# Performance work log

Measured on AMD Instinct MI355X. Metric: run time of the kernel, lower is better.

Reference implementation:

```python
import jax, jax.numpy as jnp
import numpy as np
from jax import lax

T, N, CIN, CMID, IMG, LABELS = 8, 32, 3, 64, 64, 10
W4 = IMG // 4  # 16 after two 2x2 maxpools
FC1_IN = CMID * W4 * W4                 # 16384
FC1_OUT = (CMID * W4 // 2) * W4 // 2    # 4096 (matches Python int-div precedence)
V_TH = 1.0
ALPHA = 4.0  # spikingjelly surrogate.Sigmoid default alpha

@jax.custom_vjp
def spike(x):
    # Heaviside(v - v_th); surrogate sigmoid gradient in bwd
    return (x >= 0.0).astype(x.dtype)

def _spike_fwd(x):
    return (x >= 0.0).astype(x.dtype), x

def _spike_bwd(x, g):
    s = jax.nn.sigmoid(ALPHA * x)
    return (g * ALPHA * s * (1.0 - s),)

spike.defvjp(_spike_fwd, _spike_bwd)

def if_node(x_seq):
    # IFNode, hard reset to v_reset=0, v starts at 0, multi-step over leading T axis
    def step(v, x):
        v = v + x                 # charge
        s = spike(v - V_TH)       # fire
        return v * (1.0 - s), s   # hard reset (reset path keeps grad: detach_reset=False)
    _, s_seq = lax.scan(step, jnp.zeros_like(x_seq[0]), x_seq)
    return s_seq

def conv2d(x, w):
    # kernel 3x3, stride 1, padding 1, no bias
    return lax.conv_general_dilated(x, w, (1, 1), ((1, 1), (1, 1)),
                                    dimension_numbers=('NCHW', 'OIHW', 'NCHW'))

def maxpool2(x):
    return lax.reduce_window(x, -jnp.inf, lax.max, (1, 1, 2, 2), (1, 1, 2, 2), 'VALID')

def seq_apply(f, x_seq):
    # stateless layer applied over merged [T*N, ...] (spikingjelly step_mode='m')
    t, n = x_seq.shape[:2]
    y = f(x_seq.reshape((t * n,) + x_seq.shape[2:]))
    return y.reshape((t, n) + y.shape[1:])


def setup_inputs() -> dict:
    key = jax.random.key(0)
    k = jax.random.split(key, 5)
    x_seq = jax.random.uniform(k[0], (T, N, CIN, IMG, IMG), dtype=jnp.float32)
    w1 = jax.random.normal(k[1], (CMID, CIN, 3, 3), dtype=jnp.float32) * (1.0 / np.sqrt(CIN * 9))
    w2 = jax.random.normal(k[2], (CMID, CMID, 3, 3), dtype=jnp.float32) * (1.0 / np.sqrt(CMID * 9))
    fc1 = jax.random.normal(k[3], (FC1_OUT, FC1_IN), dtype=jnp.float32) * (1.0 / np.sqrt(FC1_IN))
    fc2 = jax.random.normal(k[4], (LABELS, FC1_OUT), dtype=jnp.float32) * (1.0 / np.sqrt(FC1_OUT))
    return {"x_seq": x_seq, "w1": w1, "w2": w2, "fc1": fc1, "fc2": fc2}


def reference(x_seq, w1, w2, fc1, fc2):
    h = seq_apply(lambda x: conv2d(x, w1), x_seq)   # [T,N,64,64,64]
    h = if_node(h)
    h = seq_apply(maxpool2, h)                      # [T,N,64,32,32]
    h = seq_apply(lambda x: conv2d(x, w2), h)
    h = if_node(h)
    h = seq_apply(maxpool2, h)                      # [T,N,64,16,16]
    h = h.reshape(T, N, -1)                         # [T,N,16384]
    h = if_node(jnp.einsum('tni,oi->tno', h, fc1))  # [T,N,4096]
    h = if_node(jnp.einsum('tni,oi->tno', h, fc2))  # [T,N,10]
    return h.mean(axis=0)                           # firing rate over time: [N,10]
```

## Files before the change

### kernel.cpp

```cpp
#include <hip/hip_runtime.h>
#include <hip/hip_bf16.h>


#define T_STEPS 8
#define NB      32
#define CMID    64

typedef __bf16 bf16x2 __attribute__((ext_vector_type(2)));
typedef __bf16 bf16x4 __attribute__((ext_vector_type(4)));
typedef __bf16 bf16x8 __attribute__((ext_vector_type(8)));
typedef short  s16x8  __attribute__((ext_vector_type(8)));
typedef float  f32x4  __attribute__((ext_vector_type(4)));

struct Split3 { float h, m, l; };
__device__ __forceinline__ Split3 split3(float x) {
    Split3 s;
    __bf16 h = (__bf16)x;
    float r1 = x - (float)h;
    __bf16 m = (__bf16)r1;
    float r2 = r1 - (float)m;
    __bf16 l = (__bf16)r2;
    s.h = (float)h; s.m = (float)m; s.l = (float)l;
    return s;
}

__device__ __forceinline__ void split3v8(float4 a, float4 b,
                                         s16x8& fh, s16x8& fm, s16x8& fl) {
    float x[8] = {a.x, a.y, a.z, a.w, b.x, b.y, b.z, b.w};
    s16x8 h, m, l;
#pragma unroll
    for (int j = 0; j < 8; j++) {
        __bf16 ch = (__bf16)x[j];
        float r1 = x[j] - (float)ch;
        __bf16 cm = (__bf16)r1;
        float r2 = r1 - (float)cm;
        __bf16 cl = (__bf16)r2;
        h[j] = __builtin_bit_cast(short, ch);
        m[j] = __builtin_bit_cast(short, cm);
        l[j] = __builtin_bit_cast(short, cl);
    }
    fh = h; fm = m; fl = l;
}

__device__ __forceinline__ void load_lds16(const void* g, void* l) {
    __builtin_amdgcn_global_load_lds(
        (const __attribute__((address_space(1))) void*)g,
        (__attribute__((address_space(3))) void*)l, 16, 0, 0);
}

__global__ void k_w2s(const float* __restrict__ w2, __bf16* __restrict__ w2s) {
    int idx = blockIdx.x * 256 + threadIdx.x;
    int j    = idx & 7;
    int lane = (idx >> 3) & 63;
    int oh   = (idx >> 9) & 1;
    int kh   = (idx >> 10) & 1;
    int g    = idx >> 11;
    int tap  = g % 9;
    int ch   = g / 9;
    int co = ch * 32 + oh * 16 + (lane & 15);
    int ci = kh * 32 + (lane >> 4) * 8 + j;
    float w = w2[co * 576 + ci * 9 + tap];
    Split3 s = split3(w);
    __bf16* o = w2s + (((size_t)(g * 2 + kh) * 2 + oh) * 3) * 512 + lane * 8 + j;
    o[0]    = (__bf16)s.h;
    o[512]  = (__bf16)s.m;
    o[1024] = (__bf16)s.l;
}

__global__ __launch_bounds__(256) void k_conv1_if_pool(
        const float* __restrict__ x, const float* __restrict__ w1,
        __bf16* __restrict__ spk1p) {
    int b   = blockIdx.x;
    int n   = b >> 5;
    int cog = (b >> 2) & 7;
    int pht = b & 3;
    int tid = threadIdx.x;
    int pw  = tid & 31;
    int ph  = pht * 8 + (tid >> 5);
    int ih0 = 2 * ph - 1, iw0 = 2 * pw - 1;

    float v[8][4];
#pragma unroll
    for (int a = 0; a < 8; a++)
#pragma unroll
        for (int p = 0; p < 4; p++) v[a][p] = 0.f;

    for (int t = 0; t < T_STEPS; t++) {
        const float* xb = x + (size_t)(t * NB + n) * 3 * 4096;
        float patch[3][4][4];
#pragma unroll
        for (int ci = 0; ci < 3; ci++)
#pragma unroll
            for (int dy = 0; dy < 4; dy++) {
                int ih = ih0 + dy;
                bool rok = ((unsigned)ih < 64u);
#pragma unroll
                for (int dx = 0; dx < 4; dx++) {
                    int iw = iw0 + dx;
                    patch[ci][dy][dx] = (rok && ((unsigned)iw < 64u))
                                            ? xb[ci * 4096 + ih * 64 + iw] : 0.f;
                }
            }
        bf16x8 sv;
#pragma unroll
        for (int c8 = 0; c8 < 8; c8++) {
            int co = cog * 8 + c8;
            const float* wc = w1 + co * 27;
            float a0 = 0.f, a1 = 0.f, a2 = 0.f, a3 = 0.f;
#pragma unroll
            for (int ci = 0; ci < 3; ci++)
#pragma unroll
                for (int ky = 0; ky < 3; ky++)
#pragma unroll
                    for (int kx = 0; kx < 3; kx++) {
                        float w = wc[ci * 9 + ky * 3 + kx];
                        a0 += w * patch[ci][ky][kx];
                        a1 += w * patch[ci][ky][kx + 1];
                        a2 += w * patch[ci][ky + 1][kx];
                        a3 += w * patch[ci][ky + 1][kx + 1];
                    }
            float s0, s1, s2, s3;
            v[c8][0] += a0; s0 = (v[c8][0] >= 1.f) ? 1.f : 0.f; if (s0 > 0.f) v[c8][0] = 0.f;
            v[c8][1] += a1; s1 = (v[c8][1] >= 1.f) ? 1.f : 0.f; if (s1 > 0.f) v[c8][1] = 0.f;
            v[c8][2] += a2; s2 = (v[c8][2] >= 1.f) ? 1.f : 0.f; if (s2 > 0.f) v[c8][2] = 0.f;
            v[c8][3] += a3; s3 = (v[c8][3] >= 1.f) ? 1.f : 0.f; if (s3 > 0.f) v[c8][3] = 0.f;
            sv[c8] = (__bf16)fmaxf(fmaxf(s0, s1), fmaxf(s2, s3));
        }
        *(bf16x8*)(spk1p + ((size_t)(t * NB + n) * 1024 + ph * 32 + pw) * 64
                         + cog * 8) = sv;
    }
}

__global__ __launch_bounds__(512, 2) void k_conv2_if_pool(
        const short* __restrict__ spk1p,
        const short* __restrict__ w2s,
        __bf16* __restrict__ spk2) {
    int b     = blockIdx.x;
    int ch    = b & 1;
    int s2    = (b >> 1) & 3;
    int n     = b >> 3;
    int tid   = threadIdx.x;
    int lane  = tid & 63;
    int wv    = tid >> 6;
    int mh    = wv >> 1, oh = wv & 1;
    int lm    = lane & 15, kq = lane >> 4;

    __shared__ short Bs[55296];
    __shared__ short As[10 * 34 * 64];

    {
        const uint4* src = (const uint4*)(w2s + (size_t)ch * 55296);
        uint4* dst = (uint4*)Bs;
        for (int i = tid; i < 6912; i += 512) dst[i] = src[i];
        uint4* za = (uint4*)As;
        for (int i = tid; i < 2720; i += 512) za[i] = (uint4){0, 0, 0, 0};
    }
    __syncthreads();
    const short* Bsw = Bs + oh * 1536;

    int wl  = lane >> 3;
    int sph = lane & 7;

    f32x4 v[4];
#pragma unroll
    for (int i = 0; i < 4; i++) v[i] = (f32x4){0.f, 0.f, 0.f, 0.f};

    int co = ch * 32 + oh * 16 + lm;
    int pH = s2 * 4 + mh;

#pragma unroll 1
    for (int t = 0; t < T_STEPS; t++) {
        const short* img = spk1p + (size_t)(t * NB + n) * 65536;

        if (t > 0) __syncthreads();
#pragma unroll
        for (int q = 0; q < 5; q++) {
            int u = q * 8 + wv;
            int r = u >> 2;
            int quarter = u & 3;
            int hh = s2 * 8 - 1 + r;
            if ((unsigned)hh < 32u) {
                int widx = quarter * 8 + 1 + wl;
                int slog = sph ^ (widx & 7);
                const short* src = img + (size_t)(hh * 32 + widx - 1) * 64
                                       + slog * 8;
                short* dst = As + (r * 34 + quarter * 8 + 1) * 64;
                load_lds16(src, dst);
            }
        }
        __syncthreads();

        f32x4 acc[4];
#pragma unroll
        for (int i = 0; i < 4; i++) acc[i] = (f32x4){0.f, 0.f, 0.f, 0.f};

#pragma unroll 1
        for (int dy = 0; dy < 3; dy++) {
#pragma unroll 1
            for (int dx = 0; dx < 3; dx++) {
                const short* bp = Bsw + (dy * 3 + dx) * 6144 + lane * 8;
                s16x8 bf[2][3];
#pragma unroll
                for (int kh = 0; kh < 2; kh++)
#pragma unroll
                    for (int sp = 0; sp < 3; sp++)
                        bf[kh][sp] = *(const s16x8*)(bp + kh * 3072 + sp * 512);
#pragma unroll
                for (int i = 0; i < 4; i++) {
                    int r    = 2 * mh + (i >> 1) + dy;
                    int widx = (i & 1) * 16 + lm + dx;
                    const short* ap = As + (r * 34 + widx) * 64;
                    s16x8 a0 = *(const s16x8*)(ap + ((kq    ) ^ (widx & 7)) * 8);
                    s16x8 a1 = *(const s16x8*)(ap + ((kq + 4) ^ (widx & 7)) * 8);
#pragma unroll
                    for (int sp = 0; sp < 3; sp++) {
                        acc[i] = __builtin_amdgcn_mfma_f32_16x16x32_bf16(
                            a0, bf[0][sp], acc[i], 0, 0, 0);
                        acc[i] = __builtin_amdgcn_mfma_f32_16x16x32_bf16(
                            a1, bf[1][sp], acc[i], 0, 0, 0);
                    }
                }
            }
        }
        float s[4][4];
#pragma unroll
        for (int i = 0; i < 4; i++)
#pragma unroll
            for (int r = 0; r < 4; r++) {
                float vv = v[i][r] + acc[i][r];
                float sp = (vv >= 1.f) ? 1.f : 0.f;
                s[i][r] = sp;
                v[i][r] = (sp > 0.f) ? 0.f : vv;
            }
        __bf16* op = spk2 + ((size_t)(t * NB + n) * 64 + co) * 256 + pH * 16
                   + kq * 2;
#pragma unroll
        for (int i2 = 0; i2 < 2; i2++) {
            float p0 = fmaxf(fmaxf(s[i2][0], s[i2][1]),
                             fmaxf(s[i2 + 2][0], s[i2 + 2][1]));
            float p1 = fmaxf(fmaxf(s[i2][2], s[i2][3]),
                             fmaxf(s[i2 + 2][2], s[i2 + 2][3]));
            bf16x2 pv = {(__bf16)p0, (__bf16)p1};
            *(bf16x2*)(op + i2 * 8) = pv;
        }
    }
}

__global__ __launch_bounds__(512, 4) void k_fc1_mfma(
        const short* __restrict__ A,
        const float* __restrict__ W,
        float* __restrict__ part) {
    int b  = blockIdx.x;
    int nt = b & 63;
    int ks = b >> 6;
    int o0 = nt * 64;
    int kbase = ks * 2048;

    int tid  = threadIdx.x;
    int lane = tid & 63;
    int wv   = tid >> 6;
    int mq   = wv >> 1;
    int oh   = wv & 1;
    int lm   = lane & 15;
    int kq   = lane >> 4;

    __shared__ short Asm[2][8192];
    __shared__ float Wsm[2][2048];

    int wrow = tid >> 3;
    int wu   = (tid & 7) ^ (wrow & 7);
    const float* gW = W + (size_t)(o0 + wrow) * 16384 + kbase + wu * 4;
    const short* gA[2];
#pragma unroll
    for (int q = 0; q < 2; q++) {
        int p = q * 512 + tid;
        int r = p >> 2;
        int c = (p & 3) ^ ((r >> 1) & 3);
        gA[q] = A + (size_t)r * 16384 + kbase + c * 8;
    }

    int aoff[4];
#pragma unroll
    for (int i = 0; i < 4; i++) {
        int r = mq * 64 + i * 16 + lm;
        aoff[i] = (r * 4 + (kq ^ ((r >> 1) & 3))) * 8;
    }
    int woff[2][2];
#pragma unroll
    for (int oi = 0; oi < 2; oi++) {
        int row = (2 * oh + oi) * 16 + lm;
#pragma unroll
        for (int h = 0; h < 2; h++) {
            int u = kq * 2 + h;
            woff[oi][h] = (row * 8 + (u ^ (row & 7))) * 4;
        }
    }

    f32x4 acc[4][2];
#pragma unroll
    for (int i = 0; i < 4; i++)
#pragma unroll
        for (int oi = 0; oi < 2; oi++) acc[i][oi] = (f32x4){0.f, 0.f, 0.f, 0.f};

    load_lds16(gW, &Wsm[0][wv * 256]);
    load_lds16(gA[0], &Asm[0][wv * 512]);
    load_lds16(gA[1], &Asm[0][4096 + wv * 512]);
    __syncthreads();

#pragma unroll 1
    for (int it = 0; it < 64; ++it) {
        int bf = it & 1;
        if (it < 63) {
            load_lds16(gW + (it + 1) * 32, &Wsm[bf ^ 1][wv * 256]);
            load_lds16(gA[0] + (it + 1) * 32, &Asm[bf ^ 1][wv * 512]);
            load_lds16(gA[1] + (it + 1) * 32, &Asm[bf ^ 1][4096 + wv * 512]);
        }

        const short* as = Asm[bf];
        const float* ws = Wsm[bf];

        s16x8 av[4];
#pragma unroll
        for (int i = 0; i < 4; i++)
            av[i] = *(const s16x8*)(as + aoff[i]);

        float4 wraw[2][2];
#pragma unroll
        for (int oi = 0; oi < 2; oi++)
#pragma unroll
            for (int h = 0; h < 2; h++)
                wraw[oi][h] = *(const float4*)(ws + woff[oi][h]);

        s16x8 bfr[3][2];
#pragma unroll
        for (int oi = 0; oi < 2; oi++)
            split3v8(wraw[oi][0], wraw[oi][1],
                     bfr[0][oi], bfr[1][oi], bfr[2][oi]);

#pragma unroll
        for (int i = 0; i < 4; i++)
#pragma unroll
            for (int oi = 0; oi < 2; oi++) {
                acc[i][oi] = __builtin_amdgcn_mfma_f32_16x16x32_bf16(
                    av[i], bfr[0][oi], acc[i][oi], 0, 0, 0);
                acc[i][oi] = __builtin_amdgcn_mfma_f32_16x16x32_bf16(
                    av[i], bfr[1][oi], acc[i][oi], 0, 0, 0);
                acc[i][oi] = __builtin_amdgcn_mfma_f32_16x16x32_bf16(
                    av[i], bfr[2][oi], acc[i][oi], 0, 0, 0);
            }

        __syncthreads();
    }

    int col = lane & 15;
    int rq  = (lane >> 4) * 4;
#pragma unroll
    for (int i = 0; i < 4; i++)
#pragma unroll
        for (int oi = 0; oi < 2; oi++)
#pragma unroll
            for (int r = 0; r < 4; r++) {
                int m = mq * 64 + i * 16 + rq + r;
                int o = o0 + (2 * oh + oi) * 16 + col;
                part[((size_t)ks * 256 + m) * 4096 + o] = acc[i][oi][r];
            }
}

__global__ void k_fc1_if(const float* __restrict__ part,
                         float* __restrict__ spk3) {
    int idx = blockIdx.x * 256 + threadIdx.x;
    int o = idx & 4095;
    int n = idx >> 12;
    float v = 0.f;
    for (int t = 0; t < T_STEPS; t++) {
        int m = t * NB + n;
        float s = 0.f;
#pragma unroll
        for (int ks = 0; ks < 8; ks++)
            s += part[((size_t)ks * 256 + m) * 4096 + o];
        v += s;
        float sp = (v >= 1.f) ? 1.f : 0.f;
        if (sp > 0.f) v = 0.f;
        spk3[(size_t)m * 4096 + o] = sp;
    }
}

__global__ __launch_bounds__(256) void k_fc2_if_mean(
        const float* __restrict__ spk3, const float* __restrict__ fc2,
        float* __restrict__ out) {
    int b = blockIdx.x;
    int n = b / 10, o = b % 10;
    const float* wr = fc2 + o * 4096;
    __shared__ float red[256];
    int tid = threadIdx.x;
    float v = 0.f, cnt = 0.f;
    for (int t = 0; t < T_STEPS; t++) {
        const float* row = spk3 + (size_t)(t * NB + n) * 4096;
        float p = 0.f;
        for (int i = tid; i < 4096; i += 256) p += row[i] * wr[i];
        red[tid] = p;
        __syncthreads();
        for (int s = 128; s > 0; s >>= 1) {
            if (tid < s) red[tid] += red[tid + s];
            __syncthreads();
        }
        if (tid == 0) {
            v += red[0];
            float sp = (v >= 1.f) ? 1.f : 0.f;
            cnt += sp;
            if (sp > 0.f) v = 0.f;
        }
        __syncthreads();
    }
    if (tid == 0) out[n * 10 + o] = cnt * 0.125f;
}

extern "C" void kernel_launch(void* const* d_in, const int* in_sizes, int n_in,
                              void* d_out, int out_size, void* d_ws, size_t ws_size,
                              hipStream_t stream) {
    const float* x   = (const float*)d_in[0];
    const float* w1  = (const float*)d_in[1];
    const float* w2  = (const float*)d_in[2];
    const float* fc1 = (const float*)d_in[3];
    const float* fc2 = (const float*)d_in[4];
    float* out = (float*)d_out;

    float* ws = (float*)d_ws;
    const size_t off_w2s   = 0;
    const size_t off_spk1p = 57344;
    const size_t off_spk2  = off_spk1p + 8388608;
    const size_t off_part  = off_spk2 + 2097152;
    const size_t off_spk3  = off_part + 8388608;
    __bf16* w2s   = (__bf16*)(ws + off_w2s);
    __bf16* spk1p = (__bf16*)(ws + off_spk1p);
    __bf16* spk2  = (__bf16*)(ws + off_spk2);
    float*  part  = ws + off_part;
    float*  spk3  = ws + off_spk3;

    k_w2s<<<144, 256, 0, stream>>>(w2, w2s);
    k_conv1_if_pool<<<1024, 256, 0, stream>>>(x, w1, spk1p);
    k_conv2_if_pool<<<256, 512, 0, stream>>>((const short*)spk1p,
                                             (const short*)w2s, spk2);
    k_fc1_mfma<<<512, 512, 0, stream>>>((const short*)spk2, fc1, part);
    k_fc1_if<<<512, 256, 0, stream>>>(part, spk3);
    k_fc2_if_mean<<<320, 256, 0, stream>>>(spk3, fc2, out);
}
```

Baseline: 632.4 us.

## Triple-buffer fc1 MFMA LDS pipeline with partial vmcnt waits

Moves the fc1 MFMA kernel's LDS staging from double to triple buffering, so loads are issued two iterations ahead. The full __syncthreads wait is replaced by s_waitcnt vmcnt(3) plus a raw barrier, which lets the next tile's loads stay in flight while the current tile is computed. This is meant to hide global-load latency better. The cost is 50% more LDS per block (about 72KB), which may cut blocks per CU below the launch-bounds target of 4.

```diff
diff --git a/kernel.cpp b/kernel.cpp
--- a/kernel.cpp
+++ b/kernel.cpp
@@ -264,8 +264,8 @@
     int lm   = lane & 15;
     int kq   = lane >> 4;
 
-    __shared__ short Asm[2][8192];
-    __shared__ float Wsm[2][2048];
+    __shared__ short Asm[3][8192];
+    __shared__ float Wsm[3][2048];
 
     int wrow = tid >> 3;
     int wu   = (tid & 7) ^ (wrow & 7);
@@ -302,22 +302,28 @@
 #pragma unroll
         for (int oi = 0; oi < 2; oi++) acc[i][oi] = (f32x4){0.f, 0.f, 0.f, 0.f};
 
-    load_lds16(gW, &Wsm[0][wv * 256]);
-    load_lds16(gA[0], &Asm[0][wv * 512]);
-    load_lds16(gA[1], &Asm[0][4096 + wv * 512]);
-    __syncthreads();
+    load_lds16(gW,         &Wsm[0][wv * 256]);
+    load_lds16(gA[0],      &Asm[0][wv * 512]);
+    load_lds16(gA[1],      &Asm[0][4096 + wv * 512]);
+    load_lds16(gW + 32,    &Wsm[1][wv * 256]);
+    load_lds16(gA[0] + 32, &Asm[1][wv * 512]);
+    load_lds16(gA[1] + 32, &Asm[1][4096 + wv * 512]);
+    asm volatile("s_waitcnt vmcnt(3)" ::: "memory");
+    __builtin_amdgcn_s_barrier();
+    __builtin_amdgcn_sched_barrier(0);
 
 #pragma unroll 1
     for (int it = 0; it < 64; ++it) {
-        int bf = it & 1;
-        if (it < 63) {
-            load_lds16(gW + (it + 1) * 32, &Wsm[bf ^ 1][wv * 256]);
-            load_lds16(gA[0] + (it + 1) * 32, &Asm[bf ^ 1][wv * 512]);
-            load_lds16(gA[1] + (it + 1) * 32, &Asm[bf ^ 1][4096 + wv * 512]);
-        }
-
-        const short* as = Asm[bf];
-        const float* ws = Wsm[bf];
+        int cur = it % 3;
+        if (it < 62) {
+            int nb = (it + 2) % 3;
+            load_lds16(gW + (it + 2) * 32,    &Wsm[nb][wv * 256]);
+            load_lds16(gA[0] + (it + 2) * 32, &Asm[nb][wv * 512]);
+            load_lds16(gA[1] + (it + 2) * 32, &Asm[nb][4096 + wv * 512]);
+        }
+
+        const short* as = Asm[cur];
+        const float* ws = Wsm[cur];
 
         s16x8 av[4];
 #pragma unroll
@@ -349,7 +355,15 @@
                     av[i], bfr[2][oi], acc[i][oi], 0, 0, 0);
             }
 
-        __syncthreads();
+        if (it < 62) {
+            asm volatile("s_waitcnt vmcnt(3)" ::: "memory");
+            __builtin_amdgcn_s_barrier();
+            __builtin_amdgcn_sched_barrier(0);
+        } else if (it == 62) {
+            asm volatile("s_waitcnt vmcnt(0)" ::: "memory");
+            __builtin_amdgcn_s_barrier();
+            __builtin_amdgcn_sched_barrier(0);
+        }
     }
 
     int col = lane & 15;
```

After: 643.6 us. Within noise of the previous version (+1.8%).

## Split fc1 weights into bf16 triples once per tile and stage in LDS

Applied to the files above, without the earlier changes.

Each fp32 weight element used to be read from LDS and split into three bf16 parts by every wave that consumed it. Now each weight element is loaded from global into registers two iterations ahead, split once, and the three parts are written to a swizzled bf16 LDS buffer. Waves then read the parts directly as MFMA operands. This removes the redundant per-wave split arithmetic, at the cost of more LDS space and register-held prefetch instead of async global-to-LDS loads.

```diff
diff --git a/kernel.cpp b/kernel.cpp
--- a/kernel.cpp
+++ b/kernel.cpp
@@ -9,6 +9,7 @@
 typedef __bf16 bf16x2 __attribute__((ext_vector_type(2)));
 typedef __bf16 bf16x4 __attribute__((ext_vector_type(4)));
 typedef __bf16 bf16x8 __attribute__((ext_vector_type(8)));
+typedef short  s16x4  __attribute__((ext_vector_type(4)));
 typedef short  s16x8  __attribute__((ext_vector_type(8)));
 typedef float  f32x4  __attribute__((ext_vector_type(4)));
 
@@ -24,12 +25,12 @@
     return s;
 }
 
-__device__ __forceinline__ void split3v8(float4 a, float4 b,
-                                         s16x8& fh, s16x8& fm, s16x8& fl) {
-    float x[8] = {a.x, a.y, a.z, a.w, b.x, b.y, b.z, b.w};
-    s16x8 h, m, l;
-#pragma unroll
-    for (int j = 0; j < 8; j++) {
+__device__ __forceinline__ void split3w4(float4 v, s16x4& fh, s16x4& fm,
+                                         s16x4& fl) {
+    float x[4] = {v.x, v.y, v.z, v.w};
+    s16x4 h, m, l;
+#pragma unroll
+    for (int j = 0; j < 4; j++) {
         __bf16 ch = (__bf16)x[j];
         float r1 = x[j] - (float)ch;
         __bf16 cm = (__bf16)r1;
@@ -265,11 +266,8 @@
     int kq   = lane >> 4;
 
     __shared__ short Asm[2][8192];
-    __shared__ float Wsm[2][2048];
-
-    int wrow = tid >> 3;
-    int wu   = (tid & 7) ^ (wrow & 7);
-    const float* gW = W + (size_t)(o0 + wrow) * 16384 + kbase + wu * 4;
+    __shared__ short Wbf[2][6144];
+
     const short* gA[2];
 #pragma unroll
     for (int q = 0; q < 2; q++) {
@@ -279,21 +277,26 @@
         gA[q] = A + (size_t)r * 16384 + kbase + c * 8;
     }
 
+    int wrow = tid >> 3;
+    const float* gWf = W + (size_t)(o0 + wrow) * 16384 + kbase + (tid & 7) * 4;
+
+    {
+    }
+    int wkc   = (tid & 7) >> 1;
+    int whalf = tid & 1;
+    int wwoff = wrow * 32 + (wkc ^ ((wrow >> 1) & 3)) * 8 + whalf * 4;
+
     int aoff[4];
 #pragma unroll
     for (int i = 0; i < 4; i++) {
         int r = mq * 64 + i * 16 + lm;
         aoff[i] = (r * 4 + (kq ^ ((r >> 1) & 3))) * 8;
     }
-    int woff[2][2];
+    int wroff[2];
 #pragma unroll
     for (int oi = 0; oi < 2; oi++) {
         int row = (2 * oh + oi) * 16 + lm;
-#pragma unroll
-        for (int h = 0; h < 2; h++) {
-            int u = kq * 2 + h;
-            woff[oi][h] = (row * 8 + (u ^ (row & 7))) * 4;
-        }
+        wroff[oi] = row * 32 + (kq ^ ((row >> 1) & 3)) * 8;
     }
 
     f32x4 acc[4][2];
@@ -302,40 +305,45 @@
 #pragma unroll
         for (int oi = 0; oi < 2; oi++) acc[i][oi] = (f32x4){0.f, 0.f, 0.f, 0.f};
 
-    load_lds16(gW, &Wsm[0][wv * 256]);
+    float4 wA = *(const float4*)gWf;
     load_lds16(gA[0], &Asm[0][wv * 512]);
     load_lds16(gA[1], &Asm[0][4096 + wv * 512]);
+    {
+        s16x4 h4, m4, l4;
+        split3w4(wA, h4, m4, l4);
+        *(s16x4*)&Wbf[0][wwoff]        = h4;
+        *(s16x4*)&Wbf[0][2048 + wwoff] = m4;
+        *(s16x4*)&Wbf[0][4096 + wwoff] = l4;
+    }
+    float4 wB = *(const float4*)(gWf + 32);
     __syncthreads();
 
-#pragma unroll 1
-    for (int it = 0; it < 64; ++it) {
-        int bf = it & 1;
+    auto body = [&](int it, float4& wsplit, float4& wload) {
+        int nb = (it + 1) & 1;
         if (it < 63) {
-            load_lds16(gW + (it + 1) * 32, &Wsm[bf ^ 1][wv * 256]);
-            load_lds16(gA[0] + (it + 1) * 32, &Asm[bf ^ 1][wv * 512]);
-            load_lds16(gA[1] + (it + 1) * 32, &Asm[bf ^ 1][4096 + wv * 512]);
-        }
-
-        const short* as = Asm[bf];
-        const float* ws = Wsm[bf];
-
+            load_lds16(gA[0] + (it + 1) * 32, &Asm[nb][wv * 512]);
+            load_lds16(gA[1] + (it + 1) * 32, &Asm[nb][4096 + wv * 512]);
+            s16x4 h4, m4, l4;
+            split3w4(wsplit, h4, m4, l4);
+            *(s16x4*)&Wbf[nb][wwoff]        = h4;
+            *(s16x4*)&Wbf[nb][2048 + wwoff] = m4;
+            *(s16x4*)&Wbf[nb][4096 + wwoff] = l4;
+        }
+        if (it < 62)
+            wload = *(const float4*)(gWf + (it + 2) * 32);
+
+        const short* as = Asm[it & 1];
+        const short* wb = Wbf[it & 1];
         s16x8 av[4];
 #pragma unroll
         for (int i = 0; i < 4; i++)
             av[i] = *(const s16x8*)(as + aoff[i]);
-
-        float4 wraw[2][2];
+        s16x8 bfr[3][2];
 #pragma unroll
         for (int oi = 0; oi < 2; oi++)
 #pragma unroll
-            for (int h = 0; h < 2; h++)
-                wraw[oi][h] = *(const float4*)(ws + woff[oi][h]);
-
-        s16x8 bfr[3][2];
-#pragma unroll
-        for (int oi = 0; oi < 2; oi++)
-            split3v8(wraw[oi][0], wraw[oi][1],
-                     bfr[0][oi], bfr[1][oi], bfr[2][oi]);
+            for (int sp = 0; sp < 3; sp++)
+                bfr[sp][oi] = *(const s16x8*)(wb + sp * 2048 + wroff[oi]);
 
 #pragma unroll
         for (int i = 0; i < 4; i++)
@@ -350,6 +358,12 @@
             }
 
         __syncthreads();
+    };
+
+#pragma unroll 1
+    for (int j = 0; j < 32; ++j) {
+        body(2 * j,     wB, wA);
+        body(2 * j + 1, wA, wB);
     }
 
     int col = lane & 15;
```

Measured after the change: 628.9 us. Within noise of the previous version (-0.6%).
